# Optimization experiments

Hardware: AMD Instinct MI355X
Metric: run time of the kernel (lower is better)

## Reference

```python
import jax, jax.numpy as jnp
import numpy as np

B, S, D, H = 4, 2048, 1024, 16
DH = D // H


def setup_inputs() -> dict:
    key = jax.random.key(0)
    ks = jax.random.split(key, 5)
    scale = 0.02
    return {
        "in_features": jax.random.normal(ks[0], (B, S, D), dtype=jnp.float32),
        "Wq": jax.random.normal(ks[1], (D, D), dtype=jnp.float32) * scale,
        "Wk": jax.random.normal(ks[2], (D, D), dtype=jnp.float32) * scale,
        "Wv": jax.random.normal(ks[3], (D, D), dtype=jnp.float32) * scale,
        "Wo": jax.random.normal(ks[4], (D, D), dtype=jnp.float32) * scale,
    }


def reference(in_features, Wq, Wk, Wv, Wo):
    x = in_features  # [B, S, D]
    # projections: einsum '... s d_in, d_model d_in -> ... s d_model'  == x @ W.T
    q = jnp.einsum('bsd,md->bsm', x, Wq)
    k = jnp.einsum('bsd,md->bsm', x, Wk)
    v = jnp.einsum('bsd,md->bsm', x, Wv)
    # split heads: [B, H, S, DH]
    q = q.reshape(B, S, H, DH).transpose(0, 2, 1, 3)
    k = k.reshape(B, S, H, DH).transpose(0, 2, 1, 3)
    v = v.reshape(B, S, H, DH).transpose(0, 2, 1, 3)
    scale = 1.0 / jnp.sqrt(jnp.asarray(DH, dtype=q.dtype))
    scores = jnp.einsum('bhqd,bhkd->bhqk', q, k) * scale  # [B, H, S, S]
    causal = jnp.tril(jnp.ones((S, S), dtype=bool))
    scores = jnp.where(causal[None, None, :, :], scores, -jnp.inf)
    attn = jax.nn.softmax(scores, axis=-1)
    out = jnp.einsum('bhqk,bhkd->bhqd', attn, v)  # [B, H, S, DH]
    out = out.transpose(0, 2, 1, 3).reshape(B, S, D)
    # output projection: einsum '... s d_v, d_model d_v -> ... s d_model' == out @ Wo.T
    return jnp.einsum('bsd,md->bsm', out, Wo)
```

## Files before the change

kernel.cpp:

```cpp
#include <hip/hip_runtime.h>

typedef unsigned short u16;
typedef unsigned int u32;
typedef __attribute__((ext_vector_type(8))) short bf16x8;
typedef __attribute__((ext_vector_type(4))) short bf16x4;
typedef __attribute__((ext_vector_type(4))) float f32x4;

#define S_LEN 2048
#define NHEAD 16
#define DHEAD 64
#define DMODEL 1024

__device__ __forceinline__ u16 f2bf(float f) {
  unsigned u = __builtin_bit_cast(unsigned, f);
  unsigned r = (u + 0x7fffu + ((u >> 16) & 1u)) >> 16;
  return (u16)r;
}

__device__ __forceinline__ void gld_lds16(const void* g, void* l) {
  __builtin_amdgcn_global_load_lds((const __attribute__((address_space(1))) unsigned*)g,
                                   (__attribute__((address_space(3))) unsigned*)l,
                                   16, 0, 0);
}

__global__ void cast_all_kernel(const float* __restrict__ x,
                                const float* __restrict__ Wq, const float* __restrict__ Wk,
                                const float* __restrict__ Wv, const float* __restrict__ Wo,
                                u16* __restrict__ out) {
  int id = blockIdx.x * 256 + threadIdx.x;
  const float* s;
  int j;
  if (id < 2097152) {
    s = x; j = id;
  } else {
    int wid = id - 2097152;
    int wsel = wid >> 18;
    j = wid & 262143;
    s = wsel < 2 ? (wsel == 0 ? Wq : Wk) : (wsel == 2 ? Wv : Wo);
  }
  float4 v = reinterpret_cast<const float4*>(s)[j];
  ushort4 o;
  o.x = f2bf(v.x); o.y = f2bf(v.y); o.z = f2bf(v.z); o.w = f2bf(v.w);
  reinterpret_cast<ushort4*>(out)[id] = o;
}

__global__ __launch_bounds__(256) void gemm_qkv(const u16* __restrict__ A, const u16* __restrict__ Bw,
                                                u16* __restrict__ Qb) {
  __shared__ u16 lA[2][128 * 32];
  __shared__ u16 lB[2][128 * 32];
  const int hw = blockIdx.x;
  const int xcd = hw & 7, vv = hw >> 3;
  const int by = xcd * 8 + (vv & 7);
  const int bx = vv >> 3;
  const int tid = threadIdx.x;
  const int w = tid >> 6, lane = tid & 63;
  const int wm = w >> 1, wn = w & 1;
  const int c = lane & 15, qr = lane >> 4;
  const int brow = by * 128, bcol = bx * 128;
  f32x4 acc[4][4];
#pragma unroll
  for (int m = 0; m < 4; ++m)
#pragma unroll
    for (int n = 0; n < 4; ++n) acc[m][n] = (f32x4){0.f, 0.f, 0.f, 0.f};

  auto stage = [&](int kt, int bsel) {
    const int k0 = kt * 32;
#pragma unroll
    for (int i = 0; i < 2; ++i) {
      int slot = i * 256 + w * 64 + lane;
      int r = slot >> 2, sg = slot & 3;
      gld_lds16(A + (size_t)(brow + r) * DMODEL + k0 + sg * 8, &lA[bsel][(i * 256 + w * 64) * 8]);
      gld_lds16(Bw + (size_t)(bcol + r) * DMODEL + k0 + sg * 8, &lB[bsel][(i * 256 + w * 64) * 8]);
    }
  };

  stage(0, 0);
  __syncthreads();
  int cur = 0;
  for (int kt = 0; kt < 32; ++kt) {
    if (kt < 31) stage(kt + 1, cur ^ 1);
    bf16x8 af[4], bfr[4];
#pragma unroll
    for (int m = 0; m < 4; ++m) af[m] = *(const bf16x8*)(&lA[cur][(wm * 64 + m * 16 + c) * 32 + qr * 8]);
#pragma unroll
    for (int n = 0; n < 4; ++n) bfr[n] = *(const bf16x8*)(&lB[cur][(wn * 64 + n * 16 + c) * 32 + qr * 8]);
    __builtin_amdgcn_s_setprio(1);
#pragma unroll
    for (int m = 0; m < 4; ++m)
#pragma unroll
      for (int n = 0; n < 4; ++n)
        acc[m][n] = __builtin_amdgcn_mfma_f32_16x16x32_bf16(af[m], bfr[n], acc[m][n], 0, 0, 0);
    __builtin_amdgcn_s_setprio(0);
    __syncthreads();
    cur ^= 1;
  }

  u16* Kb = Qb + 8388608;
  u16* Vt = Kb + 8388608;
#pragma unroll
  for (int m = 0; m < 4; ++m) {
#pragma unroll
    for (int n = 0; n < 4; ++n) {
      f32x4 a = acc[m][n];
      int gm0 = brow + wm * 64 + m * 16 + qr * 4;
      int gn = bcol + wn * 64 + n * 16 + c;
      int mat = gn >> 10, gl = gn & 1023;
      int hh = gl >> 6, dh = gl & 63;
      int b = gm0 >> 11;
      if (mat == 2) {
        int s0 = gm0 & 2047;
        ushort4 pk;
        pk.x = f2bf(a[0]); pk.y = f2bf(a[1]); pk.z = f2bf(a[2]); pk.w = f2bf(a[3]);
        *reinterpret_cast<ushort4*>(Vt + ((size_t)(b * NHEAD + hh) * DHEAD + dh) * S_LEN + s0) = pk;
      } else {
        float scale = (mat == 0) ? 0.1803368801111204f : 1.0f;
        u16* dst = (mat == 0) ? Qb : Kb;
#pragma unroll
        for (int r = 0; r < 4; ++r) {
          int gm = gm0 + r;
          int s = gm & 2047;
          dst[((size_t)(b * NHEAD + hh) * S_LEN + s) * DHEAD + dh] = f2bf(a[r] * scale);
        }
      }
    }
  }
}

__global__ __launch_bounds__(256) void gemm_bt(const u16* __restrict__ A, const u16* __restrict__ Bw,
                                               float* __restrict__ outp) {
  __shared__ u16 lA[2][128 * 32];
  __shared__ u16 lB[2][128 * 32];
  const int hw = blockIdx.x;
  const int xcd = hw & 7, vv = hw >> 3;
  const int bx = vv >> 3, by = xcd * 8 + (vv & 7);
  const int tid = threadIdx.x;
  const int w = tid >> 6, lane = tid & 63;
  const int wm = w >> 1, wn = w & 1;
  const int c = lane & 15, qr = lane >> 4;
  const int brow = by * 128, bcol = bx * 128;
  f32x4 acc[4][4];
#pragma unroll
  for (int m = 0; m < 4; ++m)
#pragma unroll
    for (int n = 0; n < 4; ++n) acc[m][n] = (f32x4){0.f, 0.f, 0.f, 0.f};

  auto stage = [&](int kt, int bsel) {
    const int k0 = kt * 32;
#pragma unroll
    for (int i = 0; i < 2; ++i) {
      int slot = i * 256 + w * 64 + lane;
      int r = slot >> 2, sg = slot & 3;
      gld_lds16(A + (size_t)(brow + r) * DMODEL + k0 + sg * 8, &lA[bsel][(i * 256 + w * 64) * 8]);
      gld_lds16(Bw + (size_t)(bcol + r) * DMODEL + k0 + sg * 8, &lB[bsel][(i * 256 + w * 64) * 8]);
    }
  };

  stage(0, 0);
  __syncthreads();
  int cur = 0;
  for (int kt = 0; kt < 32; ++kt) {
    if (kt < 31) stage(kt + 1, cur ^ 1);
    bf16x8 af[4], bfr[4];
#pragma unroll
    for (int m = 0; m < 4; ++m) af[m] = *(const bf16x8*)(&lA[cur][(wm * 64 + m * 16 + c) * 32 + qr * 8]);
#pragma unroll
    for (int n = 0; n < 4; ++n) bfr[n] = *(const bf16x8*)(&lB[cur][(wn * 64 + n * 16 + c) * 32 + qr * 8]);
    __builtin_amdgcn_s_setprio(1);
#pragma unroll
    for (int m = 0; m < 4; ++m)
#pragma unroll
      for (int n = 0; n < 4; ++n)
        acc[m][n] = __builtin_amdgcn_mfma_f32_16x16x32_bf16(af[m], bfr[n], acc[m][n], 0, 0, 0);
    __builtin_amdgcn_s_setprio(0);
    __syncthreads();
    cur ^= 1;
  }

  const int rb = qr * 4;
#pragma unroll
  for (int m = 0; m < 4; ++m)
#pragma unroll
    for (int n = 0; n < 4; ++n) {
      f32x4 a = acc[m][n];
      int gm0 = brow + wm * 64 + m * 16 + rb;
      int gn = bcol + wn * 64 + n * 16 + c;
#pragma unroll
      for (int r = 0; r < 4; ++r) outp[(size_t)(gm0 + r) * DMODEL + gn] = a[r];
    }
}

__global__ __launch_bounds__(512, 4) void attn_kernel(const u16* __restrict__ Q, const u16* __restrict__ K,
                                                      const u16* __restrict__ Vt, u16* __restrict__ O) {
  __shared__ u16 lsK[2][64 * 64];
  __shared__ u16 lsV[2][64 * 64];
  __shared__ u16 lsP[8][16 * 64];
  const int x = blockIdx.x;
  const int xcd = x & 7, v = x >> 3;
  const int by = xcd * 8 + (v & 7);
  const int g = 15 - (v >> 3);
  const int tid = threadIdx.x;
  const int w = tid >> 6, lane = tid & 63;
  const int c = lane & 15, qr = lane >> 4;
  const int b = by >> 4, h = by & 15;
  u16* lp = lsP[w];

  const int q0 = g * 128 + w * 16;
  const int nd = 2 * g + (w >> 2);
  const int ntiles = 2 * g + 2;

  const u16* qrow = Q + ((size_t)by * S_LEN + q0 + c) * DHEAD;
  const bf16x8 aQ0 = *(const bf16x8*)(qrow + qr * 8);
  const bf16x8 aQ1 = *(const bf16x8*)(qrow + 32 + qr * 8);

  f32x4 o_acc[4];
#pragma unroll
  for (int d = 0; d < 4; ++d) o_acc[d] = (f32x4){0.f, 0.f, 0.f, 0.f};
  float l_run = 0.f;

  auto stage = [&](int kt, int bsel) {
    const int kv0 = kt * 64;
    int r = tid >> 3, p = tid & 7;
    int ps = p ^ (r & 7);
    gld_lds16(K + ((size_t)by * S_LEN + kv0 + r) * DHEAD + ps * 8, &lsK[bsel][(w * 64) * 8]);
    gld_lds16(Vt + ((size_t)by * DHEAD + r) * S_LEN + kv0 + ps * 8, &lsV[bsel][(w * 64) * 8]);
  };

  auto process = [&](const u16* bK, const u16* bV, int kt) {
    const int kv0 = kt * 64;
    f32x4 sc[4];
    __builtin_amdgcn_s_setprio(1);
#pragma unroll
    for (int nt = 0; nt < 4; ++nt) {
      int row = nt * 16 + c;
      const bf16x8 k0 = *(const bf16x8*)(bK + row * 64 + ((qr ^ (row & 7)) * 8));
      const bf16x8 k1 = *(const bf16x8*)(bK + row * 64 + (((4 + qr) ^ (row & 7)) * 8));
      f32x4 z = (f32x4){0.f, 0.f, 0.f, 0.f};
      z = __builtin_amdgcn_mfma_f32_16x16x32_bf16(k0, aQ0, z, 0, 0, 0);
      z = __builtin_amdgcn_mfma_f32_16x16x32_bf16(k1, aQ1, z, 0, 0, 0);
      sc[nt] = z;
    }
    __builtin_amdgcn_s_setprio(0);

    if (kt == nd) {
#pragma unroll
      for (int nt = 0; nt < 4; ++nt)
#pragma unroll
        for (int r = 0; r < 4; ++r) {
          int k_g = kv0 + nt * 16 + qr * 4 + r;
          int q_g = q0 + c;
          if (k_g > q_g) sc[nt][r] = -1e30f;
        }
    }

    float rs = 0.f;
#pragma unroll
    for (int nt = 0; nt < 4; ++nt) {
      float p0 = __builtin_amdgcn_exp2f(sc[nt][0]);
      float p1 = __builtin_amdgcn_exp2f(sc[nt][1]);
      float p2 = __builtin_amdgcn_exp2f(sc[nt][2]);
      float p3 = __builtin_amdgcn_exp2f(sc[nt][3]);
      rs += (p0 + p1) + (p2 + p3);
      u32 w01 = __builtin_amdgcn_perm(__builtin_bit_cast(u32, p1), __builtin_bit_cast(u32, p0), 0x07060302u);
      u32 w23 = __builtin_amdgcn_perm(__builtin_bit_cast(u32, p3), __builtin_bit_cast(u32, p2), 0x07060302u);
      uint2 pk; pk.x = w01; pk.y = w23;
      *reinterpret_cast<uint2*>(lp + c * 64 + (((nt * 4 + qr) ^ c) * 4)) = pk;
    }
    l_run += rs;

    bf16x8 pb[2];
#pragma unroll
    for (int ks = 0; ks < 2; ++ks) {
      bf16x4 lo = *(const bf16x4*)(lp + c * 64 + (((ks * 8 + qr * 2) ^ c) * 4));
      bf16x4 hi = *(const bf16x4*)(lp + c * 64 + (((ks * 8 + qr * 2 + 1) ^ c) * 4));
      pb[ks] = (bf16x8){lo[0], lo[1], lo[2], lo[3], hi[0], hi[1], hi[2], hi[3]};
    }
    __builtin_amdgcn_s_setprio(1);
#pragma unroll
    for (int dt = 0; dt < 4; ++dt) {
      int rowv = dt * 16 + c;
#pragma unroll
      for (int ks = 0; ks < 2; ++ks) {
        const bf16x8 vb = *(const bf16x8*)(bV + rowv * 64 + (((ks * 4 + qr) ^ (rowv & 7)) * 8));
        o_acc[dt] = __builtin_amdgcn_mfma_f32_16x16x32_bf16(vb, pb[ks], o_acc[dt], 0, 0, 0);
      }
    }
    __builtin_amdgcn_s_setprio(0);
  };

  stage(0, 0);
  __syncthreads();
  for (int kt = 0; kt < ntiles; kt += 2) {
    if (kt + 1 < ntiles) stage(kt + 1, 1);
    if (kt <= nd) process(lsK[0], lsV[0], kt);
    __syncthreads();
    if (kt + 2 < ntiles) stage(kt + 2, 0);
    if (kt + 1 <= nd) process(lsK[1], lsV[1], kt + 1);
    __syncthreads();
  }

  {
    l_run += __shfl_xor(l_run, 16);
    l_run += __shfl_xor(l_run, 32);
    float rl = 1.0f / l_run;
    int s = q0 + c;
#pragma unroll
    for (int dt = 0; dt < 4; ++dt) {
      ushort4 ok;
#pragma unroll
      for (int r = 0; r < 4; ++r) ((u16*)&ok)[r] = f2bf(o_acc[dt][r] * rl);
      *reinterpret_cast<ushort4*>(O + (((size_t)b * S_LEN + s) * NHEAD + h) * DHEAD + dt * 16 + qr * 4) = ok;
    }
  }
}

extern "C" void kernel_launch(void* const* d_in, const int* in_sizes, int n_in,
                              void* d_out, int out_size, void* d_ws, size_t ws_size,
                              hipStream_t stream) {
  (void)in_sizes; (void)n_in; (void)out_size; (void)ws_size;
  const float* x  = (const float*)d_in[0];
  const float* Wq = (const float*)d_in[1];
  const float* Wk = (const float*)d_in[2];
  const float* Wv = (const float*)d_in[3];
  const float* Wo = (const float*)d_in[4];

  u16* ws  = (u16*)d_ws;
  u16* xb  = ws;
  u16* wqb = xb  + 8388608;
  u16* wob = wqb + 3145728;
  u16* Qb  = wqb + 4194304;
  u16* Kb  = Qb  + 8388608;
  u16* Vt  = Kb  + 8388608;
  u16* Ob  = Vt  + 8388608;

  cast_all_kernel<<<12288, 256, 0, stream>>>(x, Wq, Wk, Wv, Wo, xb);

  gemm_qkv<<<1536, 256, 0, stream>>>(xb, wqb, Qb);
  attn_kernel<<<1024, 512, 0, stream>>>(Qb, Kb, Vt, Ob);
  gemm_bt<<<512, 256, 0, stream>>>(Ob, wob, (float*)d_out);
}
```

Measured before the change: 163.8 us.

## Swizzle GEMM LDS tiles and stage QKV epilogue through shared memory

Applies an XOR swizzle to the 16-byte column groups of the LDS tiles in both GEMM kernels. The swizzle is applied on the global source address for global_load_lds and undone on the fragment reads, to reduce LDS bank conflicts. The QKV GEMM epilogue now writes results into a padded shared-memory tile and then emits 16-byte coalesced stores to the head-split Q/K and transposed V layouts, replacing scattered 2-byte and 8-byte stores. The cost is an extra barrier plus a larger shared allocation that reuses the staging buffer.

```diff
diff --git a/kernel.cpp b/kernel.cpp
--- a/kernel.cpp
+++ b/kernel.cpp
@@ -46,8 +46,9 @@
 
 __global__ __launch_bounds__(256) void gemm_qkv(const u16* __restrict__ A, const u16* __restrict__ Bw,
                                                 u16* __restrict__ Qb) {
-  __shared__ u16 lA[2][128 * 32];
-  __shared__ u16 lB[2][128 * 32];
+  __shared__ u16 smem[17408];
+  u16* lA = smem;
+  u16* lB = smem + 8192;
   const int hw = blockIdx.x;
   const int xcd = hw & 7, vv = hw >> 3;
   const int by = xcd * 8 + (vv & 7);
@@ -57,6 +58,7 @@
   const int wm = w >> 1, wn = w & 1;
   const int c = lane & 15, qr = lane >> 4;
   const int brow = by * 128, bcol = bx * 128;
+  const int sw = (qr ^ ((c >> 1) & 3)) * 8;
   f32x4 acc[4][4];
 #pragma unroll
   for (int m = 0; m < 4; ++m)
@@ -69,8 +71,9 @@
     for (int i = 0; i < 2; ++i) {
       int slot = i * 256 + w * 64 + lane;
       int r = slot >> 2, sg = slot & 3;
-      gld_lds16(A + (size_t)(brow + r) * DMODEL + k0 + sg * 8, &lA[bsel][(i * 256 + w * 64) * 8]);
-      gld_lds16(Bw + (size_t)(bcol + r) * DMODEL + k0 + sg * 8, &lB[bsel][(i * 256 + w * 64) * 8]);
+      int sgs = sg ^ ((r >> 1) & 3);
+      gld_lds16(A + (size_t)(brow + r) * DMODEL + k0 + sgs * 8, lA + bsel * 4096 + (i * 256 + w * 64) * 8);
+      gld_lds16(Bw + (size_t)(bcol + r) * DMODEL + k0 + sgs * 8, lB + bsel * 4096 + (i * 256 + w * 64) * 8);
     }
   };
 
@@ -81,9 +84,9 @@
     if (kt < 31) stage(kt + 1, cur ^ 1);
     bf16x8 af[4], bfr[4];
 #pragma unroll
-    for (int m = 0; m < 4; ++m) af[m] = *(const bf16x8*)(&lA[cur][(wm * 64 + m * 16 + c) * 32 + qr * 8]);
-#pragma unroll
-    for (int n = 0; n < 4; ++n) bfr[n] = *(const bf16x8*)(&lB[cur][(wn * 64 + n * 16 + c) * 32 + qr * 8]);
+    for (int m = 0; m < 4; ++m) af[m] = *(const bf16x8*)(lA + cur * 4096 + (wm * 64 + m * 16 + c) * 32 + sw);
+#pragma unroll
+    for (int n = 0; n < 4; ++n) bfr[n] = *(const bf16x8*)(lB + cur * 4096 + (wn * 64 + n * 16 + c) * 32 + sw);
     __builtin_amdgcn_s_setprio(1);
 #pragma unroll
     for (int m = 0; m < 4; ++m)
@@ -97,31 +100,55 @@
 
   u16* Kb = Qb + 8388608;
   u16* Vt = Kb + 8388608;
-#pragma unroll
-  for (int m = 0; m < 4; ++m) {
-#pragma unroll
-    for (int n = 0; n < 4; ++n) {
-      f32x4 a = acc[m][n];
-      int gm0 = brow + wm * 64 + m * 16 + qr * 4;
-      int gn = bcol + wn * 64 + n * 16 + c;
-      int mat = gn >> 10, gl = gn & 1023;
-      int hh = gl >> 6, dh = gl & 63;
-      int b = gm0 >> 11;
-      if (mat == 2) {
-        int s0 = gm0 & 2047;
+  const int mat = bcol >> 10;
+  const int batch = by >> 4;
+  const int sbase = brow & 2047;
+  const int hbase = (bcol & 1023) >> 6;
+  u16* ep = smem;
+
+  if (mat == 2) {
+#pragma unroll
+    for (int mt = 0; mt < 4; ++mt)
+#pragma unroll
+      for (int nt = 0; nt < 4; ++nt) {
+        int n = wn * 64 + nt * 16 + c;
+        int m0 = wm * 64 + mt * 16 + qr * 4;
         ushort4 pk;
-        pk.x = f2bf(a[0]); pk.y = f2bf(a[1]); pk.z = f2bf(a[2]); pk.w = f2bf(a[3]);
-        *reinterpret_cast<ushort4*>(Vt + ((size_t)(b * NHEAD + hh) * DHEAD + dh) * S_LEN + s0) = pk;
-      } else {
-        float scale = (mat == 0) ? 0.1803368801111204f : 1.0f;
-        u16* dst = (mat == 0) ? Qb : Kb;
-#pragma unroll
-        for (int r = 0; r < 4; ++r) {
-          int gm = gm0 + r;
-          int s = gm & 2047;
-          dst[((size_t)(b * NHEAD + hh) * S_LEN + s) * DHEAD + dh] = f2bf(a[r] * scale);
-        }
+        pk.x = f2bf(acc[mt][nt][0]); pk.y = f2bf(acc[mt][nt][1]);
+        pk.z = f2bf(acc[mt][nt][2]); pk.w = f2bf(acc[mt][nt][3]);
+        *reinterpret_cast<ushort4*>(ep + n * 136 + m0) = pk;
       }
+    __syncthreads();
+#pragma unroll
+    for (int i = 0; i < 8; ++i) {
+      int id = i * 256 + tid;
+      int n = id >> 4, mch = id & 15;
+      int head = hbase + (n >> 6), dh = n & 63;
+      uint4 v4 = *reinterpret_cast<const uint4*>(ep + n * 136 + mch * 8);
+      *reinterpret_cast<uint4*>(Vt + ((size_t)(batch * NHEAD + head) * DHEAD + dh) * S_LEN + sbase + mch * 8) = v4;
+    }
+  } else {
+    float scale = (mat == 0) ? 0.1803368801111204f : 1.0f;
+    u16* dst = (mat == 0) ? Qb : Kb;
+#pragma unroll
+    for (int mt = 0; mt < 4; ++mt)
+#pragma unroll
+      for (int nt = 0; nt < 4; ++nt) {
+        int n = wn * 64 + nt * 16 + c;
+        int m0 = wm * 64 + mt * 16 + qr * 4;
+#pragma unroll
+        for (int r = 0; r < 4; ++r)
+          ep[(m0 + r) * 136 + n] = f2bf(acc[mt][nt][r] * scale);
+      }
+    __syncthreads();
+#pragma unroll
+    for (int i = 0; i < 8; ++i) {
+      int id = i * 256 + tid;
+      int m = id >> 4, hh = (id >> 3) & 1, ch = id & 7;
+      int head = hbase + hh;
+      int s = sbase + m;
+      uint4 v4 = *reinterpret_cast<const uint4*>(ep + m * 136 + hh * 64 + ch * 8);
+      *reinterpret_cast<uint4*>(dst + ((size_t)(batch * NHEAD + head) * S_LEN + s) * DHEAD + ch * 8) = v4;
     }
   }
 }
@@ -138,6 +165,7 @@
   const int wm = w >> 1, wn = w & 1;
   const int c = lane & 15, qr = lane >> 4;
   const int brow = by * 128, bcol = bx * 128;
+  const int sw = (qr ^ ((c >> 1) & 3)) * 8;
   f32x4 acc[4][4];
 #pragma unroll
   for (int m = 0; m < 4; ++m)
@@ -150,8 +178,9 @@
     for (int i = 0; i < 2; ++i) {
       int slot = i * 256 + w * 64 + lane;
       int r = slot >> 2, sg = slot & 3;
-      gld_lds16(A + (size_t)(brow + r) * DMODEL + k0 + sg * 8, &lA[bsel][(i * 256 + w * 64) * 8]);
-      gld_lds16(Bw + (size_t)(bcol + r) * DMODEL + k0 + sg * 8, &lB[bsel][(i * 256 + w * 64) * 8]);
+      int sgs = sg ^ ((r >> 1) & 3);
+      gld_lds16(A + (size_t)(brow + r) * DMODEL + k0 + sgs * 8, &lA[bsel][(i * 256 + w * 64) * 8]);
+      gld_lds16(Bw + (size_t)(bcol + r) * DMODEL + k0 + sgs * 8, &lB[bsel][(i * 256 + w * 64) * 8]);
     }
   };
 
@@ -162,9 +191,9 @@
     if (kt < 31) stage(kt + 1, cur ^ 1);
     bf16x8 af[4], bfr[4];
 #pragma unroll
-    for (int m = 0; m < 4; ++m) af[m] = *(const bf16x8*)(&lA[cur][(wm * 64 + m * 16 + c) * 32 + qr * 8]);
-#pragma unroll
-    for (int n = 0; n < 4; ++n) bfr[n] = *(const bf16x8*)(&lB[cur][(wn * 64 + n * 16 + c) * 32 + qr * 8]);
+    for (int m = 0; m < 4; ++m) af[m] = *(const bf16x8*)(&lA[cur][(wm * 64 + m * 16 + c) * 32 + sw]);
+#pragma unroll
+    for (int n = 0; n < 4; ++n) bfr[n] = *(const bf16x8*)(&lB[cur][(wn * 64 + n * 16 + c) * 32 + sw]);
     __builtin_amdgcn_s_setprio(1);
 #pragma unroll
     for (int m = 0; m < 4; ++m)
```

Result: no change. 163.2 us, median of 3 (-0.4%).
